# Performance work log

Hardware: AMD Instinct MI355X
Metric: run time of the kernel (lower is better)

## Reference

```python
import jax, jax.numpy as jnp
import numpy as np

N = 100_000      # nodes
E = 3_200_000    # edges
H = 32           # hidden_dim
L = 4            # num_layers
G = 1_000        # graphs in batch
F_IN = 1         # num_features
C = 2            # num_classes
BN_EPS = 1e-5


def setup_inputs() -> dict:
    key = jax.random.key(0)
    ks = jax.random.split(key, 8)
    s = 0.1  # param init scale
    x = jax.random.normal(ks[0], (N, F_IN), jnp.float32)
    edge_index = jax.random.randint(ks[1], (2, E), 0, N, dtype=jnp.int64)
    batch = jnp.sort(jax.random.randint(ks[2], (N,), 0, G, dtype=jnp.int64))
    return {
        "x": x,
        "edge_index": edge_index,
        "batch": batch,
        "W_enc": jax.random.normal(ks[3], (F_IN, H), jnp.float32) * s,
        "b_enc": jnp.zeros((H,), jnp.float32),
        "eps": jnp.zeros((L,), jnp.float32),           # GIN train_eps, init 0
        "W1": jax.random.normal(ks[4], (L, H, H), jnp.float32) * s,
        "b1": jnp.zeros((L, H), jnp.float32),
        "W2": jax.random.normal(ks[5], (L, H, H), jnp.float32) * s,
        "b2": jnp.zeros((L, H), jnp.float32),
        "gamma": jnp.ones((L, H), jnp.float32),
        "beta": jnp.zeros((L, H), jnp.float32),
        "W_cls": jax.random.normal(ks[6], (H, C), jnp.float32) * s,
        "b_cls": jnp.zeros((C,), jnp.float32),
    }


def reference(x, edge_index, batch, W_enc, b_enc, eps, W1, b1, W2, b2,
              gamma, beta, W_cls, b_cls):
    h = x @ W_enc + b_enc                      # [N, H] node encoder
    src, dst = edge_index[0], edge_index[1]    # message flow src -> dst
    for l in range(L):
        # GINConv: (1+eps)*x + sum_{j in N(i)} x_j
        agg = jax.ops.segment_sum(h[src], dst, num_segments=N)   # [N, H]
        z = (1.0 + eps[l]) * h + agg
        # 2-layer MLP
        z = jnp.maximum(z @ W1[l] + b1[l], 0.0) @ W2[l] + b2[l]
        # BatchNorm1d (training-mode batch statistics over nodes)
        mu = z.mean(axis=0)
        var = z.var(axis=0)
        z = gamma[l] * (z - mu) * jax.lax.rsqrt(var + BN_EPS) + beta[l]
        h = jnp.maximum(z, 0.0)                # ReLU (dropout = identity, eval)
    pooled = jax.ops.segment_sum(h, batch, num_segments=G)   # global_add_pool
    return pooled @ W_cls + b_cls              # [G, C]
```

## Files before the change

### kernel.cpp

```cpp
#include <hip/hip_runtime.h>

#define N_NODES 100000
#define N_EDGES 3200000
#define HD      32
#define NLAYERS 4
#define NGRAPHS 1000
#define BN_EPS  1e-5f
#define BSHIFT  9
#define NBUCK   ((N_NODES + 511) >> 9)
#define PCHUNK  8192
#define NPB     ((N_EDGES + PCHUNK - 1) / PCHUNK)
#define ZBLOCKS ((NGRAPHS * HD + 255) / 256)

typedef _Float16 f16;
typedef _Float16 f16x8 __attribute__((ext_vector_type(8)));
typedef float    f32x4 __attribute__((ext_vector_type(4)));
typedef int      i32x4 __attribute__((ext_vector_type(4)));
typedef unsigned int  u32x2 __attribute__((ext_vector_type(2)));
typedef unsigned char uc8 __attribute__((ext_vector_type(8)));

__global__ __launch_bounds__(256) void k_encphist(
    const int* __restrict__ ei, float* __restrict__ stats,
    float* __restrict__ pooled, int* __restrict__ pcnt)
{
    __shared__ int hist[256];
    int bb = blockIdx.x, t = threadIdx.x;
    if (bb < NPB) {
        hist[t] = 0;
        __syncthreads();
        int base4 = bb * (PCHUNK / 4);
        int n4 = min(PCHUNK / 4, N_EDGES / 4 - base4);
        const i32x4* d4 = (const i32x4*)(ei + N_EDGES);
        for (int k = t; k < n4; k += 256) {
            i32x4 d = __builtin_nontemporal_load(d4 + base4 + k);
            atomicAdd(&hist[d.x >> BSHIFT], 1);
            atomicAdd(&hist[d.y >> BSHIFT], 1);
            atomicAdd(&hist[d.z >> BSHIFT], 1);
            atomicAdd(&hist[d.w >> BSHIFT], 1);
        }
        __syncthreads();
        pcnt[t * NPB + bb] = hist[t];
    } else {
        int gid = (bb - NPB) * 256 + t;
        if (gid < NLAYERS * 64)   stats[gid]  = 0.f;
        if (gid < NGRAPHS * HD)   pooled[gid] = 0.f;
    }
}

__global__ __launch_bounds__(512) void k_pscanA(int* __restrict__ pcnt,
                                                int* __restrict__ btot)
{
    __shared__ int sc[2][512];
    int t = threadIdx.x, b = blockIdx.x;
    int base = b * NPB;
    int v = (t < NPB) ? pcnt[base + t] : 0;
    int pp = 0;
    sc[0][t] = v;
    __syncthreads();
    for (int st = 1; st < 512; st <<= 1) {
        int x = sc[pp][t];
        if (t >= st) x += sc[pp][t - st];
        sc[pp ^ 1][t] = x;
        pp ^= 1;
        __syncthreads();
    }
    int incl = sc[pp][t];
    if (t < NPB) pcnt[base + t] = incl - v;
    if (t == NPB - 1) btot[b] = incl;
}

__global__ __launch_bounds__(256) void k_pscatter(const int* __restrict__ ei,
                                                  const int* __restrict__ pcnt,
                                                  const int* __restrict__ btot,
                                                  unsigned int* __restrict__ ebuf)
{
    __shared__ int sb[2][256];
    __shared__ int lcur[256];
    int t = threadIdx.x, blk = blockIdx.x;
    sb[0][t] = (t < NBUCK) ? btot[t] : 0;
    __syncthreads();
    int pp = 0;
    for (int st = 1; st < 256; st <<= 1) {
        int v = sb[pp][t];
        if (t >= st) v += sb[pp][t - st];
        sb[pp ^ 1][t] = v;
        pp ^= 1;
        __syncthreads();
    }
    int bexcl = (t == 0) ? 0 : sb[pp][t - 1];
    lcur[t] = pcnt[t * NPB + blk] + bexcl;
    __syncthreads();
    int base4 = blk * (PCHUNK / 4);
    int n4 = min(PCHUNK / 4, N_EDGES / 4 - base4);
    const i32x4* s4 = (const i32x4*)ei;
    const i32x4* d4 = (const i32x4*)(ei + N_EDGES);
    for (int k = t; k < n4; k += 256) {
        i32x4 s = __builtin_nontemporal_load(s4 + base4 + k);
        i32x4 d = __builtin_nontemporal_load(d4 + base4 + k);
        int pos;
        pos = atomicAdd(&lcur[d.x >> BSHIFT], 1);
        ebuf[pos] = ((unsigned)s.x << BSHIFT) | (unsigned)(d.x & 511);
        pos = atomicAdd(&lcur[d.y >> BSHIFT], 1);
        ebuf[pos] = ((unsigned)s.y << BSHIFT) | (unsigned)(d.y & 511);
        pos = atomicAdd(&lcur[d.z >> BSHIFT], 1);
        ebuf[pos] = ((unsigned)s.z << BSHIFT) | (unsigned)(d.z & 511);
        pos = atomicAdd(&lcur[d.w >> BSHIFT], 1);
        ebuf[pos] = ((unsigned)s.w << BSHIFT) | (unsigned)(d.w & 511);
    }
}

__global__ __launch_bounds__(512) void k_bfinal(const unsigned int* __restrict__ ebuf,
                                                const int* __restrict__ btot,
                                                int* __restrict__ off,
                                                int* __restrict__ csr)
{
    __shared__ int sb[2][256];
    __shared__ int cnt[512], scanbuf[2][512], cur[512];
    int tid = threadIdx.x, b = blockIdx.x;
    if (tid < 256) sb[0][tid] = (tid < NBUCK) ? btot[tid] : 0;
    __syncthreads();
    int pp = 0;
    for (int st = 1; st < 256; st <<= 1) {
        if (tid < 256) {
            int v = sb[pp][tid];
            if (tid >= st) v += sb[pp][tid - st];
            sb[pp ^ 1][tid] = v;
        }
        pp ^= 1;
        __syncthreads();
    }
    int base = (b == 0) ? 0 : sb[pp][b - 1];
    int nE = sb[pp][b] - base;
    if (b == NBUCK - 1 && tid == 0) off[N_NODES] = sb[pp][NBUCK - 1];
    cnt[tid] = 0;
    __syncthreads();
    for (int e = tid; e < nE; e += 512)
        atomicAdd(&cnt[ebuf[base + e] & 511], 1);
    __syncthreads();
    int p2 = 0;
    scanbuf[0][tid] = cnt[tid];
    __syncthreads();
    for (int st = 1; st < 512; st <<= 1) {
        int v = scanbuf[p2][tid];
        if (tid >= st) v += scanbuf[p2][tid - st];
        scanbuf[p2 ^ 1][tid] = v;
        p2 ^= 1;
        __syncthreads();
    }
    int excl = scanbuf[p2][tid] - cnt[tid];
    cur[tid] = excl;
    int gnode = (b << BSHIFT) + tid;
    if (gnode < N_NODES) off[gnode] = base + excl;
    __syncthreads();
    for (int e = tid; e < nE; e += 512) {
        unsigned int p = ebuf[base + e];
        int pos = atomicAdd(&cur[p & 511], 1);
        csr[base + pos] = (int)(p >> BSHIFT);
    }
}

__global__ __launch_bounds__(256) void k_fused(
    const unsigned char* __restrict__ hq, const float* __restrict__ x,
    const int* __restrict__ off, const int* __restrict__ csr,
    const float* __restrict__ epsArr, const float* __restrict__ gamma,
    const float* __restrict__ beta, const float* __restrict__ W_enc,
    const float* __restrict__ b_enc, const float* __restrict__ W1,
    const float* __restrict__ b1, const float* __restrict__ W2,
    const float* __restrict__ b2, f16* __restrict__ z2out,
    float* __restrict__ stats, int layer)
{
    __shared__ f16 AT[4][16][5][8];
    __shared__ float T[4][16 * 36];
    __shared__ float redS[4][32], redQ[4][32];
    int tid = threadIdx.x, wave = tid >> 6, lane = tid & 63;
    int col = lane & 15, quad = lane >> 4;
    int unit = tid >> 2, li = tid & 3, ul = unit & 15;
    int node = blockIdx.x * 64 + unit;
    bool valid = node < N_NODES;
    int co = li * 8;

    f16x8 r;
    #pragma unroll
    for (int k = 0; k < 8; ++k) r[k] = (f16)0.f;

    if (valid) {
        if (layer == 0) {
            int j0 = off[node], jend = off[node + 1];
            float S = 0.f;
            for (int j = j0 + li; j < jend; j += 4) S += x[csr[j]];
            S += __shfl_xor(S, 1);
            S += __shfl_xor(S, 2);
            float oneEps = 1.f + epsArr[0];
            float u  = oneEps * x[node] + S;
            float dv = oneEps + (float)(jend - j0);
            #pragma unroll
            for (int k = 0; k < 8; ++k)
                r[k] = (f16)(fmaf(u, W_enc[co + k], dv * b_enc[co + k]));
        } else {
            float dq_s[8];
            #pragma unroll
            for (int k = 0; k < 8; ++k) {
                int ch = co + k;
                float g  = gamma[(layer - 1) * 32 + ch];
                float bb = beta[(layer - 1) * 32 + ch];
                float vmax = fmaxf(bb + 5.5f * fabsf(g), 0.f);
                dq_s[k] = fmaxf(vmax, 1e-6f) / 255.f;
            }
            float oneEps = 1.f + epsArr[layer];
            const unsigned MASK = 0x00FF00FFu;
            int j = off[node], jend = off[node + 1];
            unsigned a0 = 0, a1 = 0, a2 = 0, a3 = 0;
            auto accum = [&](u32x2 v) {
                a0 += v.x & MASK; a1 += (v.x >> 8) & MASK;
                a2 += v.y & MASK; a3 += (v.y >> 8) & MASK;
            };
            while (j < jend && (j & 3))
                accum(*(const u32x2*)(hq + csr[j++] * 32 + co));
            int n8 = (jend - j) >> 3;
            for (int it = 0; it < n8; ++it) {
                i32x4 q0 = __builtin_nontemporal_load((const i32x4*)(csr + j));
                i32x4 q1 = __builtin_nontemporal_load((const i32x4*)(csr + j + 4));
                u32x2 g0 = *(const u32x2*)(hq + q0.x * 32 + co);
                u32x2 g1 = *(const u32x2*)(hq + q0.y * 32 + co);
                u32x2 g2 = *(const u32x2*)(hq + q0.z * 32 + co);
                u32x2 g3 = *(const u32x2*)(hq + q0.w * 32 + co);
                u32x2 g4 = *(const u32x2*)(hq + q1.x * 32 + co);
                u32x2 g5 = *(const u32x2*)(hq + q1.y * 32 + co);
                u32x2 g6 = *(const u32x2*)(hq + q1.z * 32 + co);
                u32x2 g7 = *(const u32x2*)(hq + q1.w * 32 + co);
                accum(g0); accum(g1); accum(g2); accum(g3);
                accum(g4); accum(g5); accum(g6); accum(g7);
                j += 8;
            }
            if (jend - j >= 4) {
                i32x4 q0 = *(const i32x4*)(csr + j);
                accum(*(const u32x2*)(hq + q0.x * 32 + co));
                accum(*(const u32x2*)(hq + q0.y * 32 + co));
                accum(*(const u32x2*)(hq + q0.z * 32 + co));
                accum(*(const u32x2*)(hq + q0.w * 32 + co));
                j += 4;
            }
            while (j < jend)
                accum(*(const u32x2*)(hq + csr[j++] * 32 + co));

            u32x2 gs = *(const u32x2*)(hq + node * 32 + co);
            float F[8];
            F[0] = (float)(a0 & 0xFFFF); F[2] = (float)(a0 >> 16);
            F[1] = (float)(a1 & 0xFFFF); F[3] = (float)(a1 >> 16);
            F[4] = (float)(a2 & 0xFFFF); F[6] = (float)(a2 >> 16);
            F[5] = (float)(a3 & 0xFFFF); F[7] = (float)(a3 >> 16);
            #pragma unroll
            for (int k = 0; k < 4; ++k) {
                float qsl = (float)((gs.x >> (8 * k)) & 255u);
                float qsh = (float)((gs.y >> (8 * k)) & 255u);
                r[k]     = (f16)(dq_s[k]     * (F[k]     + oneEps * qsl));
                r[k + 4] = (f16)(dq_s[k + 4] * (F[k + 4] + oneEps * qsh));
            }
        }
    }

    if (valid) *(f16x8*)&AT[wave][ul][li][0] = r;

    float sA = 0.f, qA = 0.f, sB = 0.f, qB = 0.f;
    if (valid) {
        f16x8 a = *(const f16x8*)&AT[wave][col][quad][0];
        const float* W1l = W1 + layer * 1024;
        const float* W2l = W2 + layer * 1024;
        f16x8 w1a, w1b, w2a, w2b;
        #pragma unroll
        for (int jj = 0; jj < 8; ++jj) {
            int k = quad * 8 + jj;
            w1a[jj] = (f16)W1l[k * 32 + col];
            w1b[jj] = (f16)W1l[k * 32 + col + 16];
            w2a[jj] = (f16)W2l[k * 32 + col];
            w2b[jj] = (f16)W2l[k * 32 + col + 16];
        }
        float b1a = b1[layer * 32 + col], b1b = b1[layer * 32 + col + 16];
        float b2a = b2[layer * 32 + col], b2b = b2[layer * 32 + col + 16];
        f32x4 bias1a = {b1a, b1a, b1a, b1a}, bias1b = {b1b, b1b, b1b, b1b};
        f32x4 bias2a = {b2a, b2a, b2a, b2a}, bias2b = {b2b, b2b, b2b, b2b};
        float* Tw = T[wave];

        f32x4 m0 = __builtin_amdgcn_mfma_f32_16x16x32_f16(a, w1a, bias1a, 0, 0, 0);
        f32x4 m1 = __builtin_amdgcn_mfma_f32_16x16x32_f16(a, w1b, bias1b, 0, 0, 0);
        #pragma unroll
        for (int rr = 0; rr < 4; ++rr) {
            int row = quad * 4 + rr;
            Tw[row * 36 + col]      = fmaxf(m0[rr], 0.f);
            Tw[row * 36 + col + 16] = fmaxf(m1[rr], 0.f);
        }
        f32x4 t0 = *(const f32x4*)(Tw + col * 36 + quad * 8);
        f32x4 t1 = *(const f32x4*)(Tw + col * 36 + quad * 8 + 4);
        f16x8 a2;
        #pragma unroll
        for (int k = 0; k < 4; ++k) { a2[k] = (f16)t0[k]; a2[k + 4] = (f16)t1[k]; }
        f32x4 z0 = __builtin_amdgcn_mfma_f32_16x16x32_f16(a2, w2a, bias2a, 0, 0, 0);
        f32x4 zb = __builtin_amdgcn_mfma_f32_16x16x32_f16(a2, w2b, bias2b, 0, 0, 0);
        int nb = blockIdx.x * 64 + wave * 16;
        #pragma unroll
        for (int rr = 0; rr < 4; ++rr) {
            int n2 = nb + quad * 4 + rr;
            z2out[n2 * 32 + col]      = (f16)z0[rr];
            z2out[n2 * 32 + col + 16] = (f16)zb[rr];
            sA += z0[rr]; qA += z0[rr] * z0[rr];
            sB += zb[rr]; qB += zb[rr] * zb[rr];
        }
    }

    sA += __shfl_xor(sA, 16); sA += __shfl_xor(sA, 32);
    qA += __shfl_xor(qA, 16); qA += __shfl_xor(qA, 32);
    sB += __shfl_xor(sB, 16); sB += __shfl_xor(sB, 32);
    qB += __shfl_xor(qB, 16); qB += __shfl_xor(qB, 32);
    if (lane < 16) {
        redS[wave][col] = sA; redS[wave][col + 16] = sB;
        redQ[wave][col] = qA; redQ[wave][col + 16] = qB;
    }
    __syncthreads();
    if (tid < 64) {
        int sel = tid >> 5, cc = tid & 31;
        float s = 0.f;
        #pragma unroll
        for (int w = 0; w < 4; ++w) s += sel ? redQ[w][cc] : redS[w][cc];
        atomicAdd(&stats[layer * 64 + sel * 32 + cc], s);
    }
}

__global__ __launch_bounds__(256) void k_quant(
    const f16* __restrict__ z2, const float* __restrict__ stats,
    const float* __restrict__ gamma, const float* __restrict__ beta,
    unsigned char* __restrict__ hq, int layer)
{
    int idx = blockIdx.x * 256 + threadIdx.x;
    if (idx >= N_NODES * 4) return;
    int c0 = (idx & 3) * 8;
    const float invN = 1.0f / (float)N_NODES;
    float bnsc[8], bnsh[8], inv_s[8];
    #pragma unroll
    for (int k = 0; k < 8; ++k) {
        int ch = c0 + k;
        float g = gamma[layer * 32 + ch], bb = beta[layer * 32 + ch];
        float mu  = stats[layer * 64 + ch] * invN;
        float var = stats[layer * 64 + 32 + ch] * invN - mu * mu;
        float sc = g * rsqrtf(var + BN_EPS);
        bnsc[k] = sc;
        bnsh[k] = bb - mu * sc;
        float vmax = fmaxf(bb + 5.5f * fabsf(g), 0.f);
        inv_s[k] = 255.f / fmaxf(vmax, 1e-6f);
    }
    f16x8 z = *(const f16x8*)(z2 + (size_t)idx * 8);
    uc8 r;
    #pragma unroll
    for (int k = 0; k < 8; ++k) {
        float v = fmaxf(fmaf((float)z[k], bnsc[k], bnsh[k]), 0.f);
        int q = (int)(fminf(v * inv_s[k], 255.f) + 0.5f);
        r[k] = (unsigned char)q;
    }
    __builtin_nontemporal_store(r, (uc8*)(hq + (size_t)idx * 8));
}

__global__ __launch_bounds__(256) void k_pool(const f16* __restrict__ z2,
                                              const int* __restrict__ batch,
                                              const float* __restrict__ stats,
                                              const float* __restrict__ gamma,
                                              const float* __restrict__ beta,
                                              float* __restrict__ pooled)
{
    int c = threadIdx.x & 31, slot = threadIdx.x >> 5;
    const float invN = 1.0f / (float)N_NODES;
    float mu  = stats[3 * 64 + c] * invN;
    float var = stats[3 * 64 + 32 + c] * invN - mu * mu;
    float sc = gamma[3 * 32 + c] * rsqrtf(var + BN_EPS);
    float sh = beta[3 * 32 + c] - mu * sc;
    int start = blockIdx.x * 256 + slot * 32;
    if (start >= N_NODES) return;
    int end = min(start + 32, N_NODES);
    int cur = batch[start]; float acc = 0.f;
    for (int i = start; i < end; ++i) {
        int g = batch[i];
        if (g != cur) { atomicAdd(&pooled[cur * HD + c], acc); acc = 0.f; cur = g; }
        acc += fmaxf(fmaf((float)z2[i * 32 + c], sc, sh), 0.f);
    }
    atomicAdd(&pooled[cur * HD + c], acc);
}

__global__ __launch_bounds__(256) void k_cls(const float* __restrict__ pooled,
                                             const float* __restrict__ Wc,
                                             const float* __restrict__ bc,
                                             float* __restrict__ out)
{
    int gid = blockIdx.x * 256 + threadIdx.x;
    if (gid >= NGRAPHS * 2) return;
    int g = gid >> 1, c = gid & 1;
    float s = bc[c];
    #pragma unroll
    for (int k = 0; k < 32; ++k) s = fmaf(pooled[g * 32 + k], Wc[k * 2 + c], s);
    out[gid] = s;
}

extern "C" void kernel_launch(void* const* d_in, const int* in_sizes, int n_in,
                              void* d_out, int out_size, void* d_ws, size_t ws_size,
                              hipStream_t stream)
{
    const float* x      = (const float*)d_in[0];
    const int*   ei     = (const int*)d_in[1];
    const int*   batch  = (const int*)d_in[2];
    const float* W_enc  = (const float*)d_in[3];
    const float* b_enc  = (const float*)d_in[4];
    const float* epsArr = (const float*)d_in[5];
    const float* W1     = (const float*)d_in[6];
    const float* b1     = (const float*)d_in[7];
    const float* W2     = (const float*)d_in[8];
    const float* b2     = (const float*)d_in[9];
    const float* gamma  = (const float*)d_in[10];
    const float* beta   = (const float*)d_in[11];
    const float* Wc     = (const float*)d_in[12];
    const float* bc     = (const float*)d_in[13];
    float* out = (float*)d_out;

    char* ws = (char*)d_ws;
    size_t o = 0;
    auto alloc = [&](size_t bytes) {
        char* p = ws + o;
        o += (bytes + 255) & ~(size_t)255;
        return p;
    };
    unsigned char* hq = (unsigned char*)alloc((size_t)N_NODES * 32);
    f16*   z2     = (f16*) alloc((size_t)N_NODES * 32 * 2);
    int*   csr    = (int*) alloc((size_t)N_EDGES * 4);
    unsigned int* ebuf = (unsigned int*)alloc((size_t)N_EDGES * 4);
    int*   offA   = (int*) alloc((size_t)(N_NODES + 1) * 4);
    int*   pcnt   = (int*) alloc((size_t)256 * NPB * 4);
    int*   btot   = (int*) alloc(1024);
    float* stats  = (float*)alloc(NLAYERS * 64 * 4);
    float* pooled = (float*)alloc((size_t)NGRAPHS * HD * 4);

    k_encphist<<<NPB + ZBLOCKS, 256, 0, stream>>>(ei, stats, pooled, pcnt);
    k_pscanA  <<<NBUCK, 512, 0, stream>>>(pcnt, btot);
    k_pscatter<<<NPB, 256, 0, stream>>>(ei, pcnt, btot, ebuf);
    k_bfinal  <<<NBUCK, 512, 0, stream>>>(ebuf, btot, offA, csr);

    for (int l = 0; l < NLAYERS; ++l) {
        k_fused<<<(N_NODES + 63) / 64, 256, 0, stream>>>(
            hq, x, offA, csr, epsArr, gamma, beta, W_enc, b_enc,
            W1, b1, W2, b2, z2, stats, l);
        if (l < NLAYERS - 1)
            k_quant<<<(N_NODES * 4 + 255) / 256, 256, 0, stream>>>(z2, stats,
                                                                   gamma, beta,
                                                                   hq, l);
    }
    k_pool<<<(N_NODES + 255) / 256, 256, 0, stream>>>(z2, batch, stats,
                                                      gamma, beta, pooled);
    k_cls <<<8, 256, 0, stream>>>(pooled, Wc, bc, out);
}
```

Measured before the change: 442.8 us.

## Fold layer-0 neighbor scalar sum into CSR build, deepen gather unroll

The per-destination sum of x over source neighbours is now accumulated in shared memory with float atomics inside the CSR finalize kernel and written to a usum array, so layer 0 no longer performs a separate gather over the edge list. The aggregation loop in later layers is unrolled to 16 indices per iteration to keep more gathers in flight, and the self-row load is hoisted ahead of the loop. It also adds a launch-bounds occupancy hint, moves the dequant scale computation after the loop to shorten register live ranges, and writes z2 with nontemporal stores. Shared-memory float atomics make the layer-0 sum order nondeterministic, and the added x[src] lookups extra random reads to the CSR build.

```diff
diff --git a/kernel.cpp b/kernel.cpp
--- a/kernel.cpp
+++ b/kernel.cpp
@@ -111,13 +111,17 @@
 
 __global__ __launch_bounds__(512) void k_bfinal(const unsigned int* __restrict__ ebuf,
                                                 const int* __restrict__ btot,
+                                                const float* __restrict__ x,
                                                 int* __restrict__ off,
-                                                int* __restrict__ csr)
+                                                int* __restrict__ csr,
+                                                float* __restrict__ usum)
 {
     __shared__ int sb[2][256];
     __shared__ int cnt[512], scanbuf[2][512], cur[512];
+    __shared__ float fsum[512];
     int tid = threadIdx.x, b = blockIdx.x;
     if (tid < 256) sb[0][tid] = (tid < NBUCK) ? btot[tid] : 0;
+    fsum[tid] = 0.f;
     __syncthreads();
     int pp = 0;
     for (int st = 1; st < 256; st <<= 1) {
@@ -154,20 +158,24 @@
     __syncthreads();
     for (int e = tid; e < nE; e += 512) {
         unsigned int p = ebuf[base + e];
+        int src = (int)(p >> BSHIFT);
         int pos = atomicAdd(&cur[p & 511], 1);
-        csr[base + pos] = (int)(p >> BSHIFT);
-    }
-}
-
-__global__ __launch_bounds__(256) void k_fused(
+        csr[base + pos] = src;
+        atomicAdd(&fsum[p & 511], x[src]);
+    }
+    __syncthreads();
+    if (gnode < N_NODES) usum[gnode] = fsum[tid];
+}
+
+__global__ __launch_bounds__(256, 6) void k_fused(
     const unsigned char* __restrict__ hq, const float* __restrict__ x,
-    const int* __restrict__ off, const int* __restrict__ csr,
-    const float* __restrict__ epsArr, const float* __restrict__ gamma,
-    const float* __restrict__ beta, const float* __restrict__ W_enc,
-    const float* __restrict__ b_enc, const float* __restrict__ W1,
-    const float* __restrict__ b1, const float* __restrict__ W2,
-    const float* __restrict__ b2, f16* __restrict__ z2out,
-    float* __restrict__ stats, int layer)
+    const float* __restrict__ usum, const int* __restrict__ off,
+    const int* __restrict__ csr, const float* __restrict__ epsArr,
+    const float* __restrict__ gamma, const float* __restrict__ beta,
+    const float* __restrict__ W_enc, const float* __restrict__ b_enc,
+    const float* __restrict__ W1, const float* __restrict__ b1,
+    const float* __restrict__ W2, const float* __restrict__ b2,
+    f16* __restrict__ z2out, float* __restrict__ stats, int layer)
 {
     __shared__ f16 AT[4][16][5][8];
     __shared__ float T[4][16 * 36];
@@ -186,64 +194,67 @@
     if (valid) {
         if (layer == 0) {
             int j0 = off[node], jend = off[node + 1];
-            float S = 0.f;
-            for (int j = j0 + li; j < jend; j += 4) S += x[csr[j]];
-            S += __shfl_xor(S, 1);
-            S += __shfl_xor(S, 2);
             float oneEps = 1.f + epsArr[0];
-            float u  = oneEps * x[node] + S;
+            float u  = fmaf(oneEps, x[node], usum[node]);
             float dv = oneEps + (float)(jend - j0);
             #pragma unroll
             for (int k = 0; k < 8; ++k)
                 r[k] = (f16)(fmaf(u, W_enc[co + k], dv * b_enc[co + k]));
         } else {
-            float dq_s[8];
-            #pragma unroll
-            for (int k = 0; k < 8; ++k) {
-                int ch = co + k;
-                float g  = gamma[(layer - 1) * 32 + ch];
-                float bb = beta[(layer - 1) * 32 + ch];
-                float vmax = fmaxf(bb + 5.5f * fabsf(g), 0.f);
-                dq_s[k] = fmaxf(vmax, 1e-6f) / 255.f;
-            }
-            float oneEps = 1.f + epsArr[layer];
             const unsigned MASK = 0x00FF00FFu;
             int j = off[node], jend = off[node + 1];
+            u32x2 gs = *(const u32x2*)(hq + (size_t)node * 32 + co);
             unsigned a0 = 0, a1 = 0, a2 = 0, a3 = 0;
             auto accum = [&](u32x2 v) {
                 a0 += v.x & MASK; a1 += (v.x >> 8) & MASK;
                 a2 += v.y & MASK; a3 += (v.y >> 8) & MASK;
             };
+            auto rowp = [&](int idx) {
+                return (const u32x2*)(hq + (size_t)idx * 32 + co);
+            };
             while (j < jend && (j & 3))
-                accum(*(const u32x2*)(hq + csr[j++] * 32 + co));
-            int n8 = (jend - j) >> 3;
-            for (int it = 0; it < n8; ++it) {
+                accum(*rowp(csr[j++]));
+            int nrem = jend - j;
+            while (nrem >= 16) {
                 i32x4 q0 = __builtin_nontemporal_load((const i32x4*)(csr + j));
                 i32x4 q1 = __builtin_nontemporal_load((const i32x4*)(csr + j + 4));
-                u32x2 g0 = *(const u32x2*)(hq + q0.x * 32 + co);
-                u32x2 g1 = *(const u32x2*)(hq + q0.y * 32 + co);
-                u32x2 g2 = *(const u32x2*)(hq + q0.z * 32 + co);
-                u32x2 g3 = *(const u32x2*)(hq + q0.w * 32 + co);
-                u32x2 g4 = *(const u32x2*)(hq + q1.x * 32 + co);
-                u32x2 g5 = *(const u32x2*)(hq + q1.y * 32 + co);
-                u32x2 g6 = *(const u32x2*)(hq + q1.z * 32 + co);
-                u32x2 g7 = *(const u32x2*)(hq + q1.w * 32 + co);
+                i32x4 q2 = __builtin_nontemporal_load((const i32x4*)(csr + j + 8));
+                i32x4 q3 = __builtin_nontemporal_load((const i32x4*)(csr + j + 12));
+                u32x2 g0 = *rowp(q0.x), g1 = *rowp(q0.y);
+                u32x2 g2 = *rowp(q0.z), g3 = *rowp(q0.w);
+                u32x2 g4 = *rowp(q1.x), g5 = *rowp(q1.y);
+                u32x2 g6 = *rowp(q1.z), g7 = *rowp(q1.w);
+                u32x2 g8 = *rowp(q2.x), g9 = *rowp(q2.y);
+                u32x2 gA = *rowp(q2.z), gB = *rowp(q2.w);
+                u32x2 gC = *rowp(q3.x), gD = *rowp(q3.y);
+                u32x2 gE = *rowp(q3.z), gF = *rowp(q3.w);
                 accum(g0); accum(g1); accum(g2); accum(g3);
                 accum(g4); accum(g5); accum(g6); accum(g7);
-                j += 8;
+                accum(g8); accum(g9); accum(gA); accum(gB);
+                accum(gC); accum(gD); accum(gE); accum(gF);
+                j += 16; nrem -= 16;
             }
-            if (jend - j >= 4) {
+            if (nrem >= 8) {
                 i32x4 q0 = *(const i32x4*)(csr + j);
-                accum(*(const u32x2*)(hq + q0.x * 32 + co));
-                accum(*(const u32x2*)(hq + q0.y * 32 + co));
-                accum(*(const u32x2*)(hq + q0.z * 32 + co));
-                accum(*(const u32x2*)(hq + q0.w * 32 + co));
+                i32x4 q1 = *(const i32x4*)(csr + j + 4);
+                u32x2 g0 = *rowp(q0.x), g1 = *rowp(q0.y);
+                u32x2 g2 = *rowp(q0.z), g3 = *rowp(q0.w);
+                u32x2 g4 = *rowp(q1.x), g5 = *rowp(q1.y);
+                u32x2 g6 = *rowp(q1.z), g7 = *rowp(q1.w);
+                accum(g0); accum(g1); accum(g2); accum(g3);
+                accum(g4); accum(g5); accum(g6); accum(g7);
+                j += 8; nrem -= 8;
+            }
+            if (nrem >= 4) {
+                i32x4 q0 = *(const i32x4*)(csr + j);
+                accum(*rowp(q0.x)); accum(*rowp(q0.y));
+                accum(*rowp(q0.z)); accum(*rowp(q0.w));
                 j += 4;
             }
             while (j < jend)
-                accum(*(const u32x2*)(hq + csr[j++] * 32 + co));
-
-            u32x2 gs = *(const u32x2*)(hq + node * 32 + co);
+                accum(*rowp(csr[j++]));
+
+            float oneEps = 1.f + epsArr[layer];
             float F[8];
             F[0] = (float)(a0 & 0xFFFF); F[2] = (float)(a0 >> 16);
             F[1] = (float)(a1 & 0xFFFF); F[3] = (float)(a1 >> 16);
@@ -251,10 +262,16 @@
             F[5] = (float)(a3 & 0xFFFF); F[7] = (float)(a3 >> 16);
             #pragma unroll
             for (int k = 0; k < 4; ++k) {
+                float gLo  = gamma[(layer - 1) * 32 + co + k];
+                float bLo  = beta[(layer - 1) * 32 + co + k];
+                float gHi  = gamma[(layer - 1) * 32 + co + k + 4];
+                float bHi  = beta[(layer - 1) * 32 + co + k + 4];
+                float sLo = fmaxf(fmaxf(bLo + 5.5f * fabsf(gLo), 0.f), 1e-6f) / 255.f;
+                float sHi = fmaxf(fmaxf(bHi + 5.5f * fabsf(gHi), 0.f), 1e-6f) / 255.f;
                 float qsl = (float)((gs.x >> (8 * k)) & 255u);
                 float qsh = (float)((gs.y >> (8 * k)) & 255u);
-                r[k]     = (f16)(dq_s[k]     * (F[k]     + oneEps * qsl));
-                r[k + 4] = (f16)(dq_s[k + 4] * (F[k + 4] + oneEps * qsh));
+                r[k]     = (f16)(sLo * (F[k]     + oneEps * qsl));
+                r[k + 4] = (f16)(sHi * (F[k + 4] + oneEps * qsh));
             }
         }
     }
@@ -300,8 +317,8 @@
         #pragma unroll
         for (int rr = 0; rr < 4; ++rr) {
             int n2 = nb + quad * 4 + rr;
-            z2out[n2 * 32 + col]      = (f16)z0[rr];
-            z2out[n2 * 32 + col + 16] = (f16)zb[rr];
+            __builtin_nontemporal_store((f16)z0[rr], z2out + n2 * 32 + col);
+            __builtin_nontemporal_store((f16)zb[rr], z2out + n2 * 32 + col + 16);
             sA += z0[rr]; qA += z0[rr] * z0[rr];
             sB += zb[rr]; qB += zb[rr] * zb[rr];
         }
@@ -429,6 +446,7 @@
     int*   csr    = (int*) alloc((size_t)N_EDGES * 4);
     unsigned int* ebuf = (unsigned int*)alloc((size_t)N_EDGES * 4);
     int*   offA   = (int*) alloc((size_t)(N_NODES + 1) * 4);
+    float* usum   = (float*)alloc((size_t)N_NODES * 4);
     int*   pcnt   = (int*) alloc((size_t)256 * NPB * 4);
     int*   btot   = (int*) alloc(1024);
     float* stats  = (float*)alloc(NLAYERS * 64 * 4);
@@ -437,11 +455,11 @@
     k_encphist<<<NPB + ZBLOCKS, 256, 0, stream>>>(ei, stats, pooled, pcnt);
     k_pscanA  <<<NBUCK, 512, 0, stream>>>(pcnt, btot);
     k_pscatter<<<NPB, 256, 0, stream>>>(ei, pcnt, btot, ebuf);
-    k_bfinal  <<<NBUCK, 512, 0, stream>>>(ebuf, btot, offA, csr);
+    k_bfinal  <<<NBUCK, 512, 0, stream>>>(ebuf, btot, x, offA, csr, usum);
 
     for (int l = 0; l < NLAYERS; ++l) {
         k_fused<<<(N_NODES + 63) / 64, 256, 0, stream>>>(
-            hq, x, offA, csr, epsArr, gamma, beta, W_enc, b_enc,
+            hq, x, usum, offA, csr, epsArr, gamma, beta, W_enc, b_enc,
             W1, b1, W2, b2, z2, stats, l);
         if (l < NLAYERS - 1)
             k_quant<<<(N_NODES * 4 + 255) / 256, 256, 0, stream>>>(z2, stats,
```

Measured after the change: 443.2 us. About the same (+0.1%).
